# Kernel optimization log

Hardware: AMD Instinct MI355X
Metric: run time of the kernel (lower is better)

## Reference

```python
import jax, jax.numpy as jnp
import numpy as np

N, E, D_IN, H, D = 170000, 1200000, 128, 4, 32
NEG_SLOPE = 0.2


def setup_inputs() -> dict:
    key = jax.random.key(0)
    ks = jax.random.split(key, 8)
    x = jax.random.normal(ks[0], (N, D_IN), dtype=jnp.float32)
    # xavier-normal-ish scale for linear weights
    W_embed = jax.random.normal(ks[1], (D_IN, H * D), dtype=jnp.float32) * (2.0 / (D_IN + H * D)) ** 0.5
    a_src = jax.random.normal(ks[2], (H, D), dtype=jnp.float32) * (2.0 / (1 + H * D)) ** 0.5
    a_dst = jax.random.normal(ks[3], (H, D), dtype=jnp.float32) * (2.0 / (1 + H * D)) ** 0.5
    W_lin = jax.random.normal(ks[4], (D_IN, H * D), dtype=jnp.float32) * (2.0 / (D_IN + H * D)) ** 0.5
    bias = jnp.zeros((H * D,), dtype=jnp.float32)
    src = jax.random.randint(ks[5], (E,), 0, N, dtype=jnp.int32)
    dst = jax.random.randint(ks[6], (E,), 0, N, dtype=jnp.int32)
    return {"x": x, "W_embed": W_embed, "a_src": a_src, "a_dst": a_dst,
            "W_lin": W_lin, "bias": bias, "src": src, "dst": dst}


def reference(x, W_embed, a_src, a_dst, W_lin, bias, src, dst):
    n = x.shape[0]
    # node projections: [N, H, D]
    h = (x @ W_embed).reshape(n, H, D)
    dot_src = jnp.einsum('nhd,hd->nh', h, a_src)  # [N, H]
    dot_dst = jnp.einsum('nhd,hd->nh', h, a_dst)  # [N, H]
    # edge attention logits: leaky_relu(dot_src[u] + dot_dst[v])  [E, H]
    z = dot_src[src] + dot_dst[dst]
    logit = jnp.where(z >= 0, z, NEG_SLOPE * z)
    # edge softmax over incoming edges of each destination node
    m = jax.ops.segment_max(logit, dst, num_segments=n)          # [N, H]
    e = jnp.exp(logit - m[dst])                                   # [E, H]
    denom = jax.ops.segment_sum(e, dst, num_segments=n)          # [N, H]
    prob = e / denom[dst]                                         # [E, H]
    # weighted scatter-sum aggregation: sum_e prob_e * h[src_e]
    msg = h[src] * prob[:, :, None]                               # [E, H, D]
    out = jax.ops.segment_sum(msg, dst, num_segments=n)          # [N, H, D]
    out = out.reshape(n, H * D)
    out = out + x @ W_lin
    out = out + bias[None, :]
    return out
```

## Files before the change

### kernel.cpp

```cpp
#include <hip/hip_runtime.h>
#include <hip/hip_bf16.h>

static constexpr int   N_NODES   = 170000;
static constexpr int   E_EDGES   = 1200000;
static constexpr float NEG_SLOPE = 0.2f;

typedef __attribute__((ext_vector_type(8))) short bfrag8;
typedef __attribute__((ext_vector_type(4))) float facc4;

__device__ __forceinline__ short f2bf(float f) {
    __hip_bfloat16 h = __float2bfloat16(f);
    return *reinterpret_cast<short*>(&h);
}

__global__ void wt_init_kernel(const float* __restrict__ We,
                               const float* __restrict__ Wl,
                               const float* __restrict__ a_src,
                               const float* __restrict__ a_dst,
                               short* __restrict__ WtG,
                               int* __restrict__ deg)
{
    const int t = threadIdx.x;
    if (blockIdx.x < 128) {
        const int k = blockIdx.x;
        if (t < 128) WtG[t * 128 + k] = f2bf(We[k * 128 + t]);
        else         WtG[t * 128 + k] = f2bf(Wl[k * 128 + (t - 128)]);
    } else if (blockIdx.x < 136) {
        const int idx = (blockIdx.x - 128) * 256 + t;
        if (idx < 1024) {
            const int g = idx >> 7;
            const int k = idx & 127;
            const int hh = g & 3;
            const float* av = (g < 4) ? a_src : a_dst;
            float s = 0.f;
            #pragma unroll
            for (int d = 0; d < 32; ++d)
                s += We[k * 128 + hh * 32 + d] * av[hh * 32 + d];
            WtG[(256 + g) * 128 + k] = f2bf(s);
        } else {
            const int z = idx - 1024;
            WtG[(264 + (z >> 7)) * 128 + (z & 127)] = 0;
        }
    }
    const int i = blockIdx.x * 256 + t;
    if (i < N_NODES) deg[i] = 0;
}

__global__ void hist_kernel(const int* __restrict__ dst, int* __restrict__ deg) {
    int e = blockIdx.x * blockDim.x + threadIdx.x;
    if (e < E_EDGES) atomicAdd(&deg[dst[e]], 1);
}

__global__ __launch_bounds__(256) void scan_local_kernel(
    const int* __restrict__ deg, int* __restrict__ row_ptr, int* __restrict__ bsum)
{
    __shared__ int sh[256];
    const int t = threadIdx.x;
    const int base = blockIdx.x * 1024 + t * 4;
    int v0 = (base + 0 < N_NODES) ? deg[base + 0] : 0;
    int v1 = (base + 1 < N_NODES) ? deg[base + 1] : 0;
    int v2 = (base + 2 < N_NODES) ? deg[base + 2] : 0;
    int v3 = (base + 3 < N_NODES) ? deg[base + 3] : 0;
    const int tot = v0 + v1 + v2 + v3;
    sh[t] = tot;
    __syncthreads();
    for (int off = 1; off < 256; off <<= 1) {
        int add = (t >= off) ? sh[t - off] : 0;
        __syncthreads();
        sh[t] += add;
        __syncthreads();
    }
    const int excl = sh[t] - tot;
    if (base + 0 < N_NODES) row_ptr[base + 0] = excl;
    if (base + 1 < N_NODES) row_ptr[base + 1] = excl + v0;
    if (base + 2 < N_NODES) row_ptr[base + 2] = excl + v0 + v1;
    if (base + 3 < N_NODES) row_ptr[base + 3] = excl + v0 + v1 + v2;
    if (t == 255) bsum[blockIdx.x] = sh[255];
}

__global__ __launch_bounds__(256) void scan_block_kernel(
    const int* __restrict__ bsum, int* __restrict__ boff, int nblk)
{
    __shared__ int sh[256];
    const int t = threadIdx.x;
    const int v = (t < nblk) ? bsum[t] : 0;
    sh[t] = v;
    __syncthreads();
    for (int off = 1; off < 256; off <<= 1) {
        int add = (t >= off) ? sh[t - off] : 0;
        __syncthreads();
        sh[t] += add;
        __syncthreads();
    }
    boff[t] = sh[t] - v;
}

__global__ void scan_add_kernel(int* __restrict__ row_ptr,
                                const int* __restrict__ boff,
                                int* __restrict__ fill)
{
    int i = blockIdx.x * blockDim.x + threadIdx.x;
    if (i < N_NODES) {
        int v = row_ptr[i] + boff[i >> 10];
        row_ptr[i] = v;
        fill[i] = v;
    }
    if (i == 0) row_ptr[N_NODES] = E_EDGES;
}

static constexpr int LDA = 136;

__global__ __launch_bounds__(256, 4) void mfma_gemm_kernel(
    const float* __restrict__ x,
    const short* __restrict__ WtG,
    const float* __restrict__ bias,
    short* __restrict__ hbuf,
    float* __restrict__ dsrc,
    float* __restrict__ ddst,
    float* __restrict__ outp)
{
    __shared__ short As[128 * LDA];
    const int tid  = threadIdx.x;
    const long row0 = (long)blockIdx.x * 128;

    #pragma unroll
    for (int it = 0; it < 16; ++it) {
        const int idx = it * 256 + tid;
        const int r = idx >> 5;
        const int j = idx & 31;
        const long row = row0 + r;
        float4 v = make_float4(0.f, 0.f, 0.f, 0.f);
        if (row < N_NODES) v = ((const float4*)x)[row * 32 + j];
        uint u0 = (uint)(unsigned short)f2bf(v.x) | ((uint)(unsigned short)f2bf(v.y) << 16);
        uint u1 = (uint)(unsigned short)f2bf(v.z) | ((uint)(unsigned short)f2bf(v.w) << 16);
        *(uint2*)&As[r * LDA + j * 4] = make_uint2(u0, u1);
    }
    __syncthreads();

    const int w    = tid >> 6;
    const int l    = tid & 63;
    const int col  = l & 15;
    const int quad = l >> 4;
    const int abase0 = (w * 32 + col) * LDA + quad * 8;
    const int abase1 = abase0 + 16 * LDA;

    facc4 acc[2][8];
    facc4 adot[2];

    #pragma unroll
    for (int m = 0; m < 2; ++m) {
        adot[m] = (facc4)(0.f);
        #pragma unroll
        for (int t = 0; t < 8; ++t) acc[m][t] = (facc4)(0.f);
    }

    #pragma unroll
    for (int ks = 0; ks < 4; ++ks) {
        const bfrag8 a0 = *(const bfrag8*)&As[abase0 + ks * 32];
        const bfrag8 a1 = *(const bfrag8*)&As[abase1 + ks * 32];
        #pragma unroll
        for (int t = 0; t < 8; ++t) {
            const bfrag8 b = *(const bfrag8*)&WtG[(t * 16 + col) * 128 + ks * 32 + quad * 8];
            acc[0][t] = __builtin_amdgcn_mfma_f32_16x16x32_bf16(a0, b, acc[0][t], 0, 0, 0);
            acc[1][t] = __builtin_amdgcn_mfma_f32_16x16x32_bf16(a1, b, acc[1][t], 0, 0, 0);
        }
        const bfrag8 bd = *(const bfrag8*)&WtG[(256 + col) * 128 + ks * 32 + quad * 8];
        adot[0] = __builtin_amdgcn_mfma_f32_16x16x32_bf16(a0, bd, adot[0], 0, 0, 0);
        adot[1] = __builtin_amdgcn_mfma_f32_16x16x32_bf16(a1, bd, adot[1], 0, 0, 0);
    }

    #pragma unroll
    for (int m = 0; m < 2; ++m) {
        const long rbase = row0 + w * 32 + m * 16 + quad * 4;
        #pragma unroll
        for (int r = 0; r < 4; ++r) {
            const long mm = rbase + r;
            if (mm >= N_NODES) continue;
            #pragma unroll
            for (int t = 0; t < 8; ++t)
                hbuf[mm * 128 + t * 16 + col] = f2bf(acc[m][t][r]);
            if (col < 4)      dsrc[mm * 4 + col]       = adot[m][r];
            else if (col < 8) ddst[mm * 4 + (col - 4)] = adot[m][r];
        }
    }

    #pragma unroll
    for (int m = 0; m < 2; ++m)
        #pragma unroll
        for (int t = 0; t < 8; ++t) acc[m][t] = (facc4)(0.f);

    #pragma unroll
    for (int ks = 0; ks < 4; ++ks) {
        const bfrag8 a0 = *(const bfrag8*)&As[abase0 + ks * 32];
        const bfrag8 a1 = *(const bfrag8*)&As[abase1 + ks * 32];
        #pragma unroll
        for (int t = 0; t < 8; ++t) {
            const bfrag8 b = *(const bfrag8*)&WtG[(128 + t * 16 + col) * 128 + ks * 32 + quad * 8];
            acc[0][t] = __builtin_amdgcn_mfma_f32_16x16x32_bf16(a0, b, acc[0][t], 0, 0, 0);
            acc[1][t] = __builtin_amdgcn_mfma_f32_16x16x32_bf16(a1, b, acc[1][t], 0, 0, 0);
        }
    }

    #pragma unroll
    for (int t = 0; t < 8; ++t) {
        const float bv = bias[t * 16 + col];
        #pragma unroll
        for (int m = 0; m < 2; ++m) {
            const long rbase = row0 + w * 32 + m * 16 + quad * 4;
            #pragma unroll
            for (int r = 0; r < 4; ++r) {
                const long mm = rbase + r;
                if (mm < N_NODES) outp[mm * 128 + t * 16 + col] = acc[m][t][r] + bv;
            }
        }
    }
}

__global__ void csr_place_kernel(const int* __restrict__ src,
                                 const int* __restrict__ dst,
                                 int* __restrict__ fill,
                                 int* __restrict__ srcs)
{
    int e = blockIdx.x * blockDim.x + threadIdx.x;
    if (e >= E_EDGES) return;
    const int p = atomicAdd(&fill[dst[e]], 1);
    srcs[p] = src[e];
}

__global__ __launch_bounds__(256) void agg_kernel(
    const int* __restrict__ row_ptr, const int* __restrict__ srcs,
    const float* __restrict__ dsrc, const float* __restrict__ ddst,
    const short* __restrict__ hbuf, float* __restrict__ outp)
{
    const long node = (long)blockIdx.x * 4 + (threadIdx.x >> 6);
    if (node >= N_NODES) return;
    const int lane = threadIdx.x & 63;
    const int head = lane >> 4;
    const int c2   = lane << 1;
    const int start = __builtin_amdgcn_readfirstlane(row_ptr[node]);
    const int end   = __builtin_amdgcn_readfirstlane(row_ptr[node + 1]);
    if (start == end) return;

    const float dd = ddst[node * 4 + head];

    float a0 = 0.f, a1 = 0.f, dn = 0.f;

#define EDGE_LOAD(i) \
    const int   s##i = __builtin_amdgcn_readlane(sv, k + i); \
    const float e##i = dsrc[s##i * 4 + head]; \
    const uint  h##i = *(const uint*)&hbuf[(long)s##i * 128 + c2];

#define EDGE_ACC(i) { \
    float z = e##i + dd; \
    z = (z >= 0.f) ? z : NEG_SLOPE * z; \
    float wv = __expf(z); \
    if (k + i >= chunk) wv = 0.f; \
    dn += wv; \
    a0 = fmaf(wv, __uint_as_float(h##i << 16),        a0); \
    a1 = fmaf(wv, __uint_as_float(h##i & 0xFFFF0000u), a1); }

    int j = start;
    while (j < end) {
        const int rem   = end - j;
        const int chunk = rem < 64 ? rem : 64;
        int idx = j + lane;
        if (idx > end - 1) idx = end - 1;
        const int sv = srcs[idx];
        for (int k = 0; k < chunk; k += 8) {
            EDGE_LOAD(0) EDGE_LOAD(1) EDGE_LOAD(2) EDGE_LOAD(3)
            EDGE_LOAD(4) EDGE_LOAD(5) EDGE_LOAD(6) EDGE_LOAD(7)
            EDGE_ACC(0) EDGE_ACC(1) EDGE_ACC(2) EDGE_ACC(3)
            EDGE_ACC(4) EDGE_ACC(5) EDGE_ACC(6) EDGE_ACC(7)
        }
        j += chunk;
    }
#undef EDGE_LOAD
#undef EDGE_ACC

    const float inv = 1.f / dn;
    float2* op = (float2*)&outp[node * 128 + c2];
    float2 o = *op;
    o.x += a0 * inv;
    o.y += a1 * inv;
    *op = o;
}

extern "C" void kernel_launch(void* const* d_in, const int* in_sizes, int n_in,
                              void* d_out, int out_size, void* d_ws, size_t ws_size,
                              hipStream_t stream)
{
    const float* x       = (const float*)d_in[0];
    const float* W_embed = (const float*)d_in[1];
    const float* a_src   = (const float*)d_in[2];
    const float* a_dst   = (const float*)d_in[3];
    const float* W_lin   = (const float*)d_in[4];
    const float* bias    = (const float*)d_in[5];
    const int*   src     = (const int*)d_in[6];
    const int*   dst     = (const int*)d_in[7];
    float* outp = (float*)d_out;

    char* ws = (char*)d_ws;
    short* WtG   = (short*)ws;  ws += (size_t)272 * 128 * sizeof(short);
    short* hbuf  = (short*)ws;  ws += (size_t)N_NODES * 128 * sizeof(short);
    int*   srcs  = (int*)ws;    ws += (size_t)E_EDGES * sizeof(int);
    float* dsrc  = (float*)ws;  ws += (size_t)N_NODES * 4 * sizeof(float);
    float* ddst  = (float*)ws;  ws += (size_t)N_NODES * 4 * sizeof(float);
    int*   deg   = (int*)ws;    ws += (size_t)N_NODES * sizeof(int);
    int*   fill  = (int*)ws;    ws += (size_t)N_NODES * sizeof(int);
    int*   rowp  = (int*)ws;    ws += (size_t)(N_NODES + 16) * sizeof(int);
    int*   bsum  = (int*)ws;    ws += 256 * sizeof(int);
    int*   boff  = (int*)ws;    ws += 256 * sizeof(int);

    const int SCAN_BLKS = (N_NODES + 1023) / 1024;

    wt_init_kernel<<<(N_NODES + 255) / 256, 256, 0, stream>>>(
        W_embed, W_lin, a_src, a_dst, WtG, deg);
    hist_kernel<<<(E_EDGES + 255) / 256, 256, 0, stream>>>(dst, deg);
    scan_local_kernel<<<SCAN_BLKS, 256, 0, stream>>>(deg, rowp, bsum);
    scan_block_kernel<<<1, 256, 0, stream>>>(bsum, boff, SCAN_BLKS);
    scan_add_kernel<<<(N_NODES + 255) / 256, 256, 0, stream>>>(rowp, boff, fill);

    mfma_gemm_kernel<<<(N_NODES + 127) / 128, 256, 0, stream>>>(
        x, WtG, bias, hbuf, dsrc, ddst, outp);

    csr_place_kernel<<<(E_EDGES + 255) / 256, 256, 0, stream>>>(src, dst, fill, srcs);

    agg_kernel<<<(N_NODES + 3) / 4, 256, 0, stream>>>(
        rowp, srcs, dsrc, ddst, hbuf, outp);
}
```

Before: 478.6 us.

## Stage weights in LDS and load x fragments directly into registers

```diff
diff --git a/kernel.cpp b/kernel.cpp
--- a/kernel.cpp
+++ b/kernel.cpp
@@ -108,9 +108,9 @@
     if (i == 0) row_ptr[N_NODES] = E_EDGES;
 }
 
-static constexpr int LDA = 136;
-
-__global__ __launch_bounds__(256, 4) void mfma_gemm_kernel(
+static constexpr int LDB = 136;
+
+__global__ __launch_bounds__(256, 2) void mfma_gemm_kernel(
     const float* __restrict__ x,
     const short* __restrict__ WtG,
     const float* __restrict__ bias,
@@ -119,30 +119,50 @@
     float* __restrict__ ddst,
     float* __restrict__ outp)
 {
-    __shared__ short As[128 * LDA];
+    __shared__ short Bs[272 * LDB];
     const int tid  = threadIdx.x;
     const long row0 = (long)blockIdx.x * 128;
 
     #pragma unroll
-    for (int it = 0; it < 16; ++it) {
+    for (int it = 0; it < 17; ++it) {
         const int idx = it * 256 + tid;
-        const int r = idx >> 5;
-        const int j = idx & 31;
-        const long row = row0 + r;
-        float4 v = make_float4(0.f, 0.f, 0.f, 0.f);
-        if (row < N_NODES) v = ((const float4*)x)[row * 32 + j];
-        uint u0 = (uint)(unsigned short)f2bf(v.x) | ((uint)(unsigned short)f2bf(v.y) << 16);
-        uint u1 = (uint)(unsigned short)f2bf(v.z) | ((uint)(unsigned short)f2bf(v.w) << 16);
-        *(uint2*)&As[r * LDA + j * 4] = make_uint2(u0, u1);
-    }
-    __syncthreads();
+        const int n   = idx >> 4;
+        const int kc  = (idx & 15) * 8;
+        *(int4*)&Bs[n * LDB + kc] = *(const int4*)&WtG[n * 128 + kc];
+    }
 
     const int w    = tid >> 6;
     const int l    = tid & 63;
     const int col  = l & 15;
     const int quad = l >> 4;
-    const int abase0 = (w * 32 + col) * LDA + quad * 8;
-    const int abase1 = abase0 + 16 * LDA;
+
+    long ar0 = row0 + w * 32 + col;
+    long ar1 = ar0 + 16;
+    if (ar0 > N_NODES - 1) ar0 = N_NODES - 1;
+    if (ar1 > N_NODES - 1) ar1 = N_NODES - 1;
+    const float4* xp0 = (const float4*)&x[ar0 * 128 + quad * 8];
+    const float4* xp1 = (const float4*)&x[ar1 * 128 + quad * 8];
+    float4 av[2][4][2];
+    #pragma unroll
+    for (int ks = 0; ks < 4; ++ks) {
+        av[0][ks][0] = xp0[ks * 8 + 0];
+        av[0][ks][1] = xp0[ks * 8 + 1];
+        av[1][ks][0] = xp1[ks * 8 + 0];
+        av[1][ks][1] = xp1[ks * 8 + 1];
+    }
+    bfrag8 afr[2][4];
+    #pragma unroll
+    for (int m = 0; m < 2; ++m)
+        #pragma unroll
+        for (int ks = 0; ks < 4; ++ks) {
+            bfrag8 t;
+            t[0] = f2bf(av[m][ks][0].x); t[1] = f2bf(av[m][ks][0].y);
+            t[2] = f2bf(av[m][ks][0].z); t[3] = f2bf(av[m][ks][0].w);
+            t[4] = f2bf(av[m][ks][1].x); t[5] = f2bf(av[m][ks][1].y);
+            t[6] = f2bf(av[m][ks][1].z); t[7] = f2bf(av[m][ks][1].w);
+            afr[m][ks] = t;
+        }
+    __syncthreads();
 
     facc4 acc[2][8];
     facc4 adot[2];
@@ -156,17 +176,15 @@
 
     #pragma unroll
     for (int ks = 0; ks < 4; ++ks) {
-        const bfrag8 a0 = *(const bfrag8*)&As[abase0 + ks * 32];
-        const bfrag8 a1 = *(const bfrag8*)&As[abase1 + ks * 32];
         #pragma unroll
         for (int t = 0; t < 8; ++t) {
-            const bfrag8 b = *(const bfrag8*)&WtG[(t * 16 + col) * 128 + ks * 32 + quad * 8];
-            acc[0][t] = __builtin_amdgcn_mfma_f32_16x16x32_bf16(a0, b, acc[0][t], 0, 0, 0);
-            acc[1][t] = __builtin_amdgcn_mfma_f32_16x16x32_bf16(a1, b, acc[1][t], 0, 0, 0);
-        }
-        const bfrag8 bd = *(const bfrag8*)&WtG[(256 + col) * 128 + ks * 32 + quad * 8];
-        adot[0] = __builtin_amdgcn_mfma_f32_16x16x32_bf16(a0, bd, adot[0], 0, 0, 0);
-        adot[1] = __builtin_amdgcn_mfma_f32_16x16x32_bf16(a1, bd, adot[1], 0, 0, 0);
+            const bfrag8 b = *(const bfrag8*)&Bs[(t * 16 + col) * LDB + ks * 32 + quad * 8];
+            acc[0][t] = __builtin_amdgcn_mfma_f32_16x16x32_bf16(afr[0][ks], b, acc[0][t], 0, 0, 0);
+            acc[1][t] = __builtin_amdgcn_mfma_f32_16x16x32_bf16(afr[1][ks], b, acc[1][t], 0, 0, 0);
+        }
+        const bfrag8 bd = *(const bfrag8*)&Bs[(256 + col) * LDB + ks * 32 + quad * 8];
+        adot[0] = __builtin_amdgcn_mfma_f32_16x16x32_bf16(afr[0][ks], bd, adot[0], 0, 0, 0);
+        adot[1] = __builtin_amdgcn_mfma_f32_16x16x32_bf16(afr[1][ks], bd, adot[1], 0, 0, 0);
     }
 
     #pragma unroll
@@ -191,13 +209,11 @@
 
     #pragma unroll
     for (int ks = 0; ks < 4; ++ks) {
-        const bfrag8 a0 = *(const bfrag8*)&As[abase0 + ks * 32];
-        const bfrag8 a1 = *(const bfrag8*)&As[abase1 + ks * 32];
         #pragma unroll
         for (int t = 0; t < 8; ++t) {
-            const bfrag8 b = *(const bfrag8*)&WtG[(128 + t * 16 + col) * 128 + ks * 32 + quad * 8];
-            acc[0][t] = __builtin_amdgcn_mfma_f32_16x16x32_bf16(a0, b, acc[0][t], 0, 0, 0);
-            acc[1][t] = __builtin_amdgcn_mfma_f32_16x16x32_bf16(a1, b, acc[1][t], 0, 0, 0);
+            const bfrag8 b = *(const bfrag8*)&Bs[(128 + t * 16 + col) * LDB + ks * 32 + quad * 8];
+            acc[0][t] = __builtin_amdgcn_mfma_f32_16x16x32_bf16(afr[0][ks], b, acc[0][t], 0, 0, 0);
+            acc[1][t] = __builtin_amdgcn_mfma_f32_16x16x32_bf16(afr[1][ks], b, acc[1][t], 0, 0, 0);
         }
     }
 
```

Measured after the change: 417.2 us. 12.8% less time.
